# Kernel optimization log

Hardware: AMD Instinct MI355X
Metric: run time of the kernel (lower is better)

Reference implementation:

```python
import jax, jax.numpy as jnp
import numpy as np
import math

B, P, C = 8, 65536, 21
H, Wd, A = 128, 128, 4  # P == H*Wd*A
EMB, NID = 256, 1000
RATIO = 15
EMB_SCALE = math.sqrt(2) * math.log(NID - 1)


def setup_inputs() -> dict:
    key = jax.random.key(0)
    k1, k2, k3, k4, k5, k6 = jax.random.split(key, 6)
    confidence = jax.random.normal(k1, (B, P, C), dtype=jnp.float32)
    predicted_ids = jax.random.normal(k2, (B, H, Wd, EMB), dtype=jnp.float32)
    raw = jax.random.randint(k3, (B, P), 1, C)
    is_pos = jax.random.uniform(k4, (B, P)) < 0.02
    labels = jnp.where(is_pos, raw, 0).astype(jnp.int64)
    gt_ids = jax.random.randint(k5, (B, H, Wd, A), 0, NID).astype(jnp.int64)
    W = jax.random.normal(k6, (NID, EMB), dtype=jnp.float32) * 0.02
    b = jnp.zeros((NID,), dtype=jnp.float32)
    return {"confidence": confidence, "predicted_ids": predicted_ids,
            "labels": labels, "gt_ids": gt_ids, "W": W, "b": b}


def _hard_negative_mining(bg_loss, labels, ratio):
    # bg_loss: [B,P] = -log_softmax(confidence)[:, :, 0]
    pos = labels > 0
    num_pos = pos.sum(axis=1, keepdims=True)
    num_neg = num_pos * ratio
    l = jnp.where(pos, -jnp.inf, bg_loss)
    order = jnp.argsort(-l, axis=1)          # descending loss
    ranks = jnp.argsort(order, axis=1)       # rank of each prior
    neg = ranks < num_neg
    return pos | neg                          # [B,P]


def reference(confidence, predicted_ids, labels, gt_ids, W, b):
    # --- no_grad mining over all priors ---
    bg_loss = -jax.nn.log_softmax(confidence, axis=2)[:, :, 0]
    emb_mask = _hard_negative_mining(bg_loss, labels, RATIO)        # [B,P]
    # split to feature-map layout and reduce over anchors (mask.max(3))
    loc_mask = emb_mask.reshape(gt_ids.shape).max(axis=3)           # [B,H,W] bool
    gid = gt_ids.max(axis=3)                                        # [B,H,W]

    # --- normalize + scale + linear (computed densely, selection via mask) ---
    nrm = jnp.linalg.norm(predicted_ids, axis=-1, keepdims=True)
    pid = EMB_SCALE * predicted_ids / jnp.maximum(nrm, 1e-12)       # F.normalize
    logits = jnp.einsum('bhwe,ne->bhwn', pid, W) + b                # [B,H,W,NID]

    # --- masked cross-entropy, mean over selected & gid != -1 ---
    logp = jax.nn.log_softmax(logits, axis=-1)
    gid_safe = jnp.clip(gid, 0, NID - 1)
    ce = -jnp.take_along_axis(logp, gid_safe[..., None], axis=-1)[..., 0]
    valid = loc_mask & (gid >= 0)
    vf = valid.astype(ce.dtype)
    loss = (ce * vf).sum() / jnp.maximum(vf.sum(), 1.0)
    return loss
```

## Files before the change

kernel.cpp:

```cpp
#include <hip/hip_runtime.h>

typedef unsigned long long u64;
typedef __attribute__((ext_vector_type(8))) short short8;
typedef __attribute__((ext_vector_type(4))) float f32x4;

#define NB 8
#define PP 65536
#define CC 21
#define LOC_PER_B 16384
#define EMB_SCALE_F 9.76762622f
#define NID 1000

#define OFF_KEYS   0ull
#define OFF_HIST   4194304ull
#define OFF_WSWZ   6291456ull
#define OFF_STATE  6815744ull
#define ST_NUMPOS   0
#define ST_CANDCNT  32
#define ST_KTHHI    64
#define ST_KREM     96
#define ST_DONE     128
#define ST_KTH      160
#define ST_ACCUM    224
#define ST_WORDS    58

__device__ __forceinline__ unsigned short f2bf(float f) {
    unsigned u = __float_as_uint(f);
    u = (u + 0x7FFFu + ((u >> 16) & 1u)) >> 16;
    return (unsigned short)u;
}

__device__ __forceinline__ void gl_lds16(const void* g, void* l) {
    __builtin_amdgcn_global_load_lds((const __attribute__((address_space(1))) unsigned*)g,
                                     (__attribute__((address_space(3))) unsigned*)l, 16, 0, 0);
}

__global__ void k_init(unsigned* __restrict__ hist, unsigned* __restrict__ state) {
    int idx = blockIdx.x * 256 + threadIdx.x;
    if (idx < 524288) hist[idx] = 0u;
    int t = idx - 524288;
    if (t >= 0 && t < ST_WORDS) state[t] = 0u;
}

__global__ void k_wprep(const float* __restrict__ Wm, unsigned short* __restrict__ wswz) {
    int g = blockIdx.x * 256 + threadIdx.x;
    if (g >= 32768) return;
    int c    = g & 31;
    int row  = (g >> 5) & 63;
    int tile = g >> 11;
    int cls  = tile * 64 + row;
    int srcByte = (c << 4) ^ ((row & 7) << 4);
    ushort4 h0, h1;
    if (cls < NID) {
        const float* src = Wm + (size_t)cls * 256 + (srcByte >> 1);
        float4 a = *(const float4*)(src);
        float4 b = *(const float4*)(src + 4);
        h0.x = f2bf(a.x); h0.y = f2bf(a.y); h0.z = f2bf(a.z); h0.w = f2bf(a.w);
        h1.x = f2bf(b.x); h1.y = f2bf(b.y); h1.z = f2bf(b.z); h1.w = f2bf(b.w);
    } else {
        h0.x = h0.y = h0.z = h0.w = 0;
        h1.x = h1.y = h1.z = h1.w = 0;
    }
    ushort4* dst = (ushort4*)((char*)wswz + ((size_t)g << 4));
    dst[0] = h0; dst[1] = h1;
}

__global__ void k_keys(const float* __restrict__ conf, const int* __restrict__ labels,
                       u64* __restrict__ keys, int* __restrict__ numPos,
                       unsigned* __restrict__ hist) {
    int idx = blockIdx.x * 256 + threadIdx.x;
    int b = idx >> 16;
    int p = idx & 65535;
    const float* c = conf + (size_t)idx * CC;
    float x0 = c[0];
    float m = x0;
#pragma unroll
    for (int j = 1; j < CC; ++j) m = fmaxf(m, c[j]);
    float s = 0.f;
#pragma unroll
    for (int j = 0; j < CC; ++j) s += __expf(c[j] - m);
    float bg = m + __logf(s) - x0;
    bool pos = labels[idx] > 0;
    unsigned u = __float_as_uint(bg);
    u = (u & 0x80000000u) ? ~u : (u | 0x80000000u);
    u64 key = pos ? 0ull : ((((u64)u) << 32) | (u64)(0xFFFFFFFFu - (unsigned)p));
    keys[idx] = key;
    if (key) atomicAdd(&hist[(b << 16) + (int)(key >> 48)], 1u);
    u64 bal = __ballot(pos);
    if ((threadIdx.x & 63) == 0) {
        int cnt = __popcll(bal);
        if (cnt) atomicAdd(&numPos[b], cnt);
    }
}

__global__ void k_scan0(const unsigned* __restrict__ hist, const int* __restrict__ numPos,
                        unsigned* __restrict__ kthHi, unsigned* __restrict__ kRem,
                        unsigned* __restrict__ done, u64* __restrict__ kth) {
    int b = blockIdx.x, t = threadIdx.x;
    __shared__ unsigned s[1024];
    __shared__ unsigned sh_c, sh_kk;
    int np = numPos[b];
    long long kk64 = (long long)np * 15;
    long long neg = (long long)PP - np;
    if (kk64 > neg) kk64 = neg;
    unsigned k = (unsigned)kk64;
    if (k == 0) { if (t == 0) { done[b] = 1u; kth[b] = ~0ull; } return; }
    const unsigned* h = hist + (b << 16);
    unsigned cs = 0;
    const uint4* hv = (const uint4*)(h + (t << 6));
#pragma unroll
    for (int j = 0; j < 16; ++j) { uint4 v = hv[j]; cs += v.x + v.y + v.z + v.w; }
    s[t] = cs; __syncthreads();
    for (int off = 1; off < 1024; off <<= 1) {
        unsigned v = (t + off < 1024) ? s[t + off] : 0u;
        __syncthreads(); s[t] += v; __syncthreads();
    }
    unsigned si = s[t];
    if (si >= k && si - cs < k) { sh_c = (unsigned)t; sh_kk = k - (si - cs); }
    __syncthreads();
    if (t < 64) {
        unsigned c = sh_c, kk = sh_kk;
        unsigned bin = h[(c << 6) + t];
        unsigned sfx = bin;
        for (int off = 1; off < 64; off <<= 1) {
            unsigned v = __shfl_down(sfx, off, 64);
            if (t + off < 64) sfx += v;
        }
        if (sfx >= kk && sfx - bin < kk) {
            kthHi[b] = (c << 6) | (unsigned)t;
            kRem[b]  = kk - (sfx - bin);
        }
    }
}

__global__ void k_compact(const u64* __restrict__ keys, const unsigned* __restrict__ kthHi,
                          const unsigned* __restrict__ done, u64* __restrict__ cand,
                          unsigned* __restrict__ candCnt) {
    int idx = blockIdx.x * 256 + threadIdx.x;
    int b = idx >> 16;
    if (done[b]) return;
    u64 key = keys[idx];
    if ((unsigned)(key >> 48) == kthHi[b]) {
        unsigned pos = atomicAdd(&candCnt[b], 1u);
        if (pos < 32768u) cand[((size_t)b << 15) + pos] = key;
    }
}

__global__ void k_select2(const u64* __restrict__ cand, const unsigned* __restrict__ candCnt,
                          const unsigned* __restrict__ kthHi, const unsigned* __restrict__ kRem,
                          const unsigned* __restrict__ done, u64* __restrict__ kth) {
    int b = blockIdx.x, t = threadIdx.x;
    if (done[b]) return;
    __shared__ unsigned wh[4][256];
    __shared__ unsigned s[256];
    __shared__ u64 sh_pref;
    __shared__ unsigned sh_kk;
    int wv = t >> 6;
    unsigned n = candCnt[b]; if (n > 32768u) n = 32768u;
    if (t == 0) { sh_pref = 0ull; sh_kk = kRem[b]; }
    __syncthreads();
    const u64* cb = cand + ((size_t)b << 15);
    for (int pass = 0; pass < 6; ++pass) {
        int shift = 40 - 8 * pass;
        wh[0][t] = 0u; wh[1][t] = 0u; wh[2][t] = 0u; wh[3][t] = 0u;
        __syncthreads();
        u64 pref = sh_pref; unsigned kk = sh_kk;
        u64 himask = (~((1ull << (shift + 8)) - 1ull)) & 0x0000FFFFFFFFFFFFull;
        for (unsigned i = t; i < n; i += 256) {
            u64 kv = cb[i] & 0x0000FFFFFFFFFFFFull;
            if ((kv & himask) == pref)
                atomicAdd(&wh[wv][(unsigned)(kv >> shift) & 255u], 1u);
        }
        __syncthreads();
        unsigned hsum = wh[0][t] + wh[1][t] + wh[2][t] + wh[3][t];
        s[t] = hsum; __syncthreads();
        for (int off = 1; off < 256; off <<= 1) {
            unsigned v = (t + off < 256) ? s[t + off] : 0u;
            __syncthreads(); s[t] += v; __syncthreads();
        }
        unsigned si = s[t];
        if (si >= kk && si - hsum < kk) {
            sh_pref = pref | ((u64)t << shift);
            sh_kk = kk - (si - hsum);
        }
        __syncthreads();
    }
    if (t == 0) kth[b] = ((u64)kthHi[b] << 48) | sh_pref;
}

__launch_bounds__(256, 2)
__global__ void k_ce(const float* __restrict__ pid, const int* __restrict__ labels,
                     const int* __restrict__ gt, const unsigned short* __restrict__ wswz,
                     const float* __restrict__ bias, const u64* __restrict__ keys,
                     const u64* __restrict__ kth_, const unsigned* __restrict__ done_,
                     float* __restrict__ accum) {
    __shared__ __align__(16) char Ws[65536];
    __shared__ __align__(16) float biasLds[1024];
    __shared__ int gid_s[128];
    __shared__ unsigned mask_s[128];
    __shared__ float fsum[128];
    __shared__ float fgl[128];

    int tid = threadIdx.x;
    int blk = blockIdx.x;
    int b = blk >> 7;
    int locBase = (blk & 127) << 7;
    int wv = tid >> 6, lane = tid & 63;

#pragma unroll
    for (int i = 0; i < 4; ++i) {
        int idx = tid + (i << 8);
        biasLds[idx] = (idx < NID) ? bias[idx] : -INFINITY;
    }

    const float4* Xg = (const float4*)pid + ((size_t)b * LOC_PER_B + (size_t)locBase) * 64;
    for (int it = 0; it < 32; ++it) {
        int r = (it << 2) + wv;
        float4 v = Xg[(size_t)r * 64 + lane];
        float ss = v.x * v.x + v.y * v.y + v.z * v.z + v.w * v.w;
#pragma unroll
        for (int o = 32; o >= 1; o >>= 1) ss += __shfl_xor(ss, o, 64);
        float sc = EMB_SCALE_F / fmaxf(sqrtf(ss), 1e-12f);
        ushort4 h;
        h.x = f2bf(v.x * sc); h.y = f2bf(v.y * sc);
        h.z = f2bf(v.z * sc); h.w = f2bf(v.w * sc);
        *(ushort4*)(Ws + r * 512 + (((lane << 3)) ^ ((r & 7) << 4))) = h;
    }

    if (tid < 128) {
        size_t pb = (size_t)b * PP + ((size_t)(locBase + tid) << 2);
        int g0 = gt[pb], g1 = gt[pb + 1], g2 = gt[pb + 2], g3 = gt[pb + 3];
        int gid = max(max(g0, g1), max(g2, g3));
        u64 kth = kth_[b];
        unsigned dn = done_[b];
        unsigned msk = 0;
#pragma unroll
        for (int a = 0; a < 4; ++a) {
            if (labels[pb + a] > 0 || (!dn && keys[pb + a] >= kth)) msk = 1u;
        }
        if (gid < 0) msk = 0;
        gid_s[tid] = min(max(gid, 0), NID - 1);
        mask_s[tid] = msk;
        fsum[tid] = 0.f;
        fgl[tid] = 0.f;
    }

    asm volatile("s_waitcnt lgkmcnt(0)" ::: "memory");
    asm volatile("s_barrier" ::: "memory");

    int wrow = (wv >> 1) << 5;
    int wcol = (wv & 1) << 5;
    int kb = (lane >> 4) << 4;
    short8 af[2][2][8];
#pragma unroll
    for (int p = 0; p < 2; ++p)
#pragma unroll
        for (int ci = 0; ci < 2; ++ci) {
            int r = (p << 6) + wrow + (ci << 4) + (lane & 15);
            int swz = (r & 7) << 4;
#pragma unroll
            for (int ks = 0; ks < 8; ++ks)
                af[p][ci][ks] = *(const short8*)(Ws + r * 512 + ((((ks << 6) + kb)) ^ swz));
        }
    asm volatile("s_waitcnt lgkmcnt(0)" ::: "memory");
    asm volatile("s_barrier" ::: "memory");

    const char* wg = (const char*)wswz;
    {
        const char* g0 = wg + (wv << 13) + (lane << 4);
        char* l0 = Ws + (wv << 13);
#pragma unroll
        for (int it = 0; it < 8; ++it) gl_lds16(g0 + (it << 10), l0 + (it << 10));
        const char* g1 = wg + 32768 + (wv << 13) + (lane << 4);
        char* l1 = Ws + 32768 + (wv << 13);
#pragma unroll
        for (int it = 0; it < 8; ++it) gl_lds16(g1 + (it << 10), l1 + (it << 10));
    }

    float runsum[16];
#pragma unroll
    for (int i = 0; i < 16; ++i) runsum[i] = 0.f;

    int rc0 = wcol + (lane & 15);
    int swzB = (rc0 & 7) << 4;
    int kbx = kb ^ (swzB & 48);
    int szh = swzB & 64;
    int rbase0 = rc0 * 512 + kbx;
    int rbase1 = (rc0 + 16) * 512 + kbx;

    for (int nt = 0; nt < 16; ++nt) {
        int p = nt & 1;
        if (nt < 15) asm volatile("s_waitcnt vmcnt(8)" ::: "memory");
        else         asm volatile("s_waitcnt vmcnt(0)" ::: "memory");
        asm volatile("s_barrier" ::: "memory");

        const char* Wp = Ws + (p << 15);
        f32x4 a00 = {0,0,0,0}, a01 = {0,0,0,0}, a10 = {0,0,0,0}, a11 = {0,0,0,0};
        f32x4 c00 = {0,0,0,0}, c01 = {0,0,0,0}, c10 = {0,0,0,0}, c11 = {0,0,0,0};
#pragma unroll
        for (int ks = 0; ks < 8; ++ks) {
            int o = ((ks << 6) ^ szh);
            short8 b0 = *(const short8*)(Wp + rbase0 + o);
            short8 b1 = *(const short8*)(Wp + rbase1 + o);
            a00 = __builtin_amdgcn_mfma_f32_16x16x32_bf16(af[0][0][ks], b0, a00, 0, 0, 0);
            a01 = __builtin_amdgcn_mfma_f32_16x16x32_bf16(af[0][0][ks], b1, a01, 0, 0, 0);
            a10 = __builtin_amdgcn_mfma_f32_16x16x32_bf16(af[0][1][ks], b0, a10, 0, 0, 0);
            a11 = __builtin_amdgcn_mfma_f32_16x16x32_bf16(af[0][1][ks], b1, a11, 0, 0, 0);
            c00 = __builtin_amdgcn_mfma_f32_16x16x32_bf16(af[1][0][ks], b0, c00, 0, 0, 0);
            c01 = __builtin_amdgcn_mfma_f32_16x16x32_bf16(af[1][0][ks], b1, c01, 0, 0, 0);
            c10 = __builtin_amdgcn_mfma_f32_16x16x32_bf16(af[1][1][ks], b0, c10, 0, 0, 0);
            c11 = __builtin_amdgcn_mfma_f32_16x16x32_bf16(af[1][1][ks], b1, c11, 0, 0, 0);
        }
        asm volatile("s_barrier" ::: "memory");

        if (nt < 14) {
            const char* gs = wg + ((size_t)(nt + 2) << 15) + (wv << 13) + (lane << 4);
            char* ls = Ws + (p << 15) + (wv << 13);
#pragma unroll
            for (int it = 0; it < 8; ++it) gl_lds16(gs + (it << 10), ls + (it << 10));
        }

        int n0 = nt << 6;
        float bl0 = biasLds[n0 + wcol + (lane & 15)];
        float bl1 = biasLds[n0 + wcol + 16 + (lane & 15)];
#pragma unroll
        for (int reg = 0; reg < 4; ++reg) {
            runsum[reg]      += __expf(a00[reg] + bl0) + __expf(a01[reg] + bl1);
            runsum[4 + reg]  += __expf(a10[reg] + bl0) + __expf(a11[reg] + bl1);
            runsum[8 + reg]  += __expf(c00[reg] + bl0) + __expf(c01[reg] + bl1);
            runsum[12 + reg] += __expf(c10[reg] + bl0) + __expf(c11[reg] + bl1);
        }
    }

    if ((wv & 1) == 0) {
#pragma unroll
        for (int p = 0; p < 2; ++p)
#pragma unroll
            for (int ci = 0; ci < 2; ++ci) {
                int r = (p << 6) + wrow + (ci << 4) + (lane & 15);
                int gid = gid_s[r];
                const char* wrp = (const char*)wswz + (size_t)gid * 512;
                int gswz = (gid & 7) << 4;
                float d = 0.f;
#pragma unroll
                for (int ks = 0; ks < 8; ++ks) {
                    short8 w8 = *(const short8*)(wrp + ((((ks << 6) + kb)) ^ gswz));
                    short8 a8 = af[p][ci][ks];
#pragma unroll
                    for (int j = 0; j < 8; ++j) {
                        float xa = __uint_as_float((unsigned)(unsigned short)a8[j] << 16);
                        float xw = __uint_as_float((unsigned)(unsigned short)w8[j] << 16);
                        d = fmaf(xa, xw, d);
                    }
                }
                d += __shfl_xor(d, 16, 64);
                d += __shfl_xor(d, 32, 64);
                if (lane < 16) fgl[r] = d + biasLds[gid];
            }
    }

#pragma unroll
    for (int o = 1; o <= 8; o <<= 1)
#pragma unroll
        for (int i = 0; i < 16; ++i) runsum[i] += __shfl_xor(runsum[i], o, 64);

    if ((lane & 15) == 0) {
        int rb = wrow + ((lane >> 4) << 2);
#pragma unroll
        for (int p = 0; p < 2; ++p)
#pragma unroll
            for (int reg = 0; reg < 4; ++reg) {
                atomicAdd(&fsum[(p << 6) + rb + reg],      runsum[p * 8 + reg]);
                atomicAdd(&fsum[(p << 6) + rb + 16 + reg], runsum[p * 8 + 4 + reg]);
            }
    }
    __syncthreads();

    if (tid < 128) {
        float ce = __logf(fsum[tid]) - fgl[tid];
        float mm = (float)mask_s[tid];
        float cs = ce * mm;
#pragma unroll
        for (int o = 1; o <= 32; o <<= 1) {
            cs += __shfl_xor(cs, o, 64);
            mm += __shfl_xor(mm, o, 64);
        }
        if (lane == 0) {
            atomicAdd(&accum[0], cs);
            atomicAdd(&accum[1], mm);
        }
    }
}

__global__ void k_fin(const float* __restrict__ accum, float* __restrict__ out) {
    out[0] = accum[0] / fmaxf(accum[1], 1.0f);
}

extern "C" void kernel_launch(void* const* d_in, const int* in_sizes, int n_in,
                              void* d_out, int out_size, void* d_ws, size_t ws_size,
                              hipStream_t stream) {
    (void)in_sizes; (void)n_in; (void)out_size; (void)ws_size;
    const float* conf   = (const float*)d_in[0];
    const float* pid    = (const float*)d_in[1];
    const int*   labels = (const int*)d_in[2];
    const int*   gt     = (const int*)d_in[3];
    const float* Wm     = (const float*)d_in[4];
    const float* bias   = (const float*)d_in[5];
    float* out = (float*)d_out;
    char* ws = (char*)d_ws;

    u64* keys           = (u64*)(ws + OFF_KEYS);
    unsigned* hist      = (unsigned*)(ws + OFF_HIST);
    u64* cand           = (u64*)(ws + OFF_HIST);
    unsigned short* wsw = (unsigned short*)(ws + OFF_WSWZ);
    char* st            = ws + OFF_STATE;
    int* numPos         = (int*)(st + ST_NUMPOS);
    unsigned* candCnt   = (unsigned*)(st + ST_CANDCNT);
    unsigned* kthHi     = (unsigned*)(st + ST_KTHHI);
    unsigned* kRem      = (unsigned*)(st + ST_KREM);
    unsigned* done      = (unsigned*)(st + ST_DONE);
    u64* kth            = (u64*)(st + ST_KTH);
    float* accum        = (float*)(st + ST_ACCUM);

    k_init   <<<2049, 256, 0, stream>>>(hist, (unsigned*)st);
    k_wprep  <<<128,  256, 0, stream>>>(Wm, wsw);
    k_keys   <<<2048, 256, 0, stream>>>(conf, labels, keys, numPos, hist);
    k_scan0  <<<8,   1024, 0, stream>>>(hist, numPos, kthHi, kRem, done, kth);
    k_compact<<<2048, 256, 0, stream>>>(keys, kthHi, done, cand, candCnt);
    k_select2<<<8,    256, 0, stream>>>(cand, candCnt, kthHi, kRem, done, kth);
    k_ce     <<<1024, 256, 0, stream>>>(pid, labels, gt, wsw, bias, keys, kth, done, accum);
    k_fin    <<<1, 1, 0, stream>>>(accum, out);
}
```

Before: 481.4 us.

## Restructure CE kernel tiling, fold norm scale into epilogue, stage keys input in LDS

Measured after the change: 608.0 us. 26.3% more time.

```diff
diff --git a/kernel.cpp b/kernel.cpp
--- a/kernel.cpp
+++ b/kernel.cpp
@@ -4,10 +4,8 @@
 typedef __attribute__((ext_vector_type(8))) short short8;
 typedef __attribute__((ext_vector_type(4))) float f32x4;
 
-#define NB 8
 #define PP 65536
 #define CC 21
-#define LOC_PER_B 16384
 #define EMB_SCALE_F 9.76762622f
 #define NID 1000
 
@@ -30,48 +28,57 @@
     return (unsigned short)u;
 }
 
+__device__ __forceinline__ float bf2f(short s) {
+    return __uint_as_float((unsigned)(unsigned short)s << 16);
+}
+
 __device__ __forceinline__ void gl_lds16(const void* g, void* l) {
     __builtin_amdgcn_global_load_lds((const __attribute__((address_space(1))) unsigned*)g,
                                      (__attribute__((address_space(3))) unsigned*)l, 16, 0, 0);
 }
 
-__global__ void k_init(unsigned* __restrict__ hist, unsigned* __restrict__ state) {
+__global__ void k_prep(const float* __restrict__ Wm, unsigned short* __restrict__ wswz,
+                       unsigned* __restrict__ hist, unsigned* __restrict__ state) {
     int idx = blockIdx.x * 256 + threadIdx.x;
-    if (idx < 524288) hist[idx] = 0u;
-    int t = idx - 524288;
-    if (t >= 0 && t < ST_WORDS) state[t] = 0u;
-}
-
-__global__ void k_wprep(const float* __restrict__ Wm, unsigned short* __restrict__ wswz) {
-    int g = blockIdx.x * 256 + threadIdx.x;
-    if (g >= 32768) return;
-    int c    = g & 31;
-    int row  = (g >> 5) & 63;
-    int tile = g >> 11;
-    int cls  = tile * 64 + row;
-    int srcByte = (c << 4) ^ ((row & 7) << 4);
-    ushort4 h0, h1;
-    if (cls < NID) {
-        const float* src = Wm + (size_t)cls * 256 + (srcByte >> 1);
-        float4 a = *(const float4*)(src);
-        float4 b = *(const float4*)(src + 4);
-        h0.x = f2bf(a.x); h0.y = f2bf(a.y); h0.z = f2bf(a.z); h0.w = f2bf(a.w);
-        h1.x = f2bf(b.x); h1.y = f2bf(b.y); h1.z = f2bf(b.z); h1.w = f2bf(b.w);
-    } else {
+    hist[idx] = 0u;
+    if (idx < ST_WORDS) state[idx] = 0u;
+    if (idx < 32768) {
+        int c    = idx & 31;
+        int row  = (idx >> 5) & 31;
+        int tile = idx >> 10;
+        int cls  = tile * 32 + row;
+        ushort4 h0, h1;
         h0.x = h0.y = h0.z = h0.w = 0;
         h1.x = h1.y = h1.z = h1.w = 0;
-    }
-    ushort4* dst = (ushort4*)((char*)wswz + ((size_t)g << 4));
-    dst[0] = h0; dst[1] = h1;
+        if (cls < NID) {
+            int srcByte = (c << 4) ^ ((row & 7) << 4);
+            const float* s = Wm + (size_t)cls * 256 + (srcByte >> 1);
+            float4 a = *(const float4*)s;
+            float4 b = *(const float4*)(s + 4);
+            h0.x = f2bf(a.x); h0.y = f2bf(a.y); h0.z = f2bf(a.z); h0.w = f2bf(a.w);
+            h1.x = f2bf(b.x); h1.y = f2bf(b.y); h1.z = f2bf(b.z); h1.w = f2bf(b.w);
+        }
+        ushort4* dst = (ushort4*)((char*)wswz + ((size_t)idx << 4));
+        dst[0] = h0; dst[1] = h1;
+    }
 }
 
 __global__ void k_keys(const float* __restrict__ conf, const int* __restrict__ labels,
                        u64* __restrict__ keys, int* __restrict__ numPos,
                        unsigned* __restrict__ hist) {
-    int idx = blockIdx.x * 256 + threadIdx.x;
+    __shared__ float cs[5376];
+    int tid = threadIdx.x, blk = blockIdx.x;
+    const float4* src = (const float4*)(conf + (size_t)blk * 5376);
+#pragma unroll
+    for (int it = 0; it < 6; ++it) {
+        int g = tid + (it << 8);
+        if (g < 1344) ((float4*)cs)[g] = src[g];
+    }
+    __syncthreads();
+    int idx = blk * 256 + tid;
     int b = idx >> 16;
     int p = idx & 65535;
-    const float* c = conf + (size_t)idx * CC;
+    const float* c = cs + tid * 21;
     float x0 = c[0];
     float m = x0;
 #pragma unroll
@@ -87,7 +94,7 @@
     keys[idx] = key;
     if (key) atomicAdd(&hist[(b << 16) + (int)(key >> 48)], 1u);
     u64 bal = __ballot(pos);
-    if ((threadIdx.x & 63) == 0) {
+    if ((tid & 63) == 0) {
         int cnt = __popcll(bal);
         if (cnt) atomicAdd(&numPos[b], cnt);
     }
@@ -188,16 +195,16 @@
     if (t == 0) kth[b] = ((u64)kthHi[b] << 48) | sh_pref;
 }
 
-__launch_bounds__(256, 2)
+__launch_bounds__(256, 4)
 __global__ void k_ce(const float* __restrict__ pid, const int* __restrict__ labels,
                      const int* __restrict__ gt, const unsigned short* __restrict__ wswz,
                      const float* __restrict__ bias, const u64* __restrict__ keys,
                      const u64* __restrict__ kth_, const unsigned* __restrict__ done_,
                      float* __restrict__ accum) {
-    __shared__ __align__(16) char Ws[65536];
-    __shared__ __align__(16) float biasLds[1024];
+    __shared__ __align__(16) char Ws[32768];
+    __shared__ float biasLds[1024];
     __shared__ int gid_s[128];
-    __shared__ unsigned mask_s[128];
+    __shared__ float mask_s[128];
     __shared__ float fsum[128];
     __shared__ float fgl[128];
 
@@ -206,26 +213,39 @@
     int b = blk >> 7;
     int locBase = (blk & 127) << 7;
     int wv = tid >> 6, lane = tid & 63;
-
-#pragma unroll
-    for (int i = 0; i < 4; ++i) {
-        int idx = tid + (i << 8);
-        biasLds[idx] = (idx < NID) ? bias[idx] : -INFINITY;
-    }
-
-    const float4* Xg = (const float4*)pid + ((size_t)b * LOC_PER_B + (size_t)locBase) * 64;
-    for (int it = 0; it < 32; ++it) {
-        int r = (it << 2) + wv;
-        float4 v = Xg[(size_t)r * 64 + lane];
-        float ss = v.x * v.x + v.y * v.y + v.z * v.z + v.w * v.w;
-#pragma unroll
-        for (int o = 32; o >= 1; o >>= 1) ss += __shfl_xor(ss, o, 64);
-        float sc = EMB_SCALE_F / fmaxf(sqrtf(ss), 1e-12f);
-        ushort4 h;
-        h.x = f2bf(v.x * sc); h.y = f2bf(v.y * sc);
-        h.z = f2bf(v.z * sc); h.w = f2bf(v.w * sc);
-        *(ushort4*)(Ws + r * 512 + (((lane << 3)) ^ ((r & 7) << 4))) = h;
-    }
+    int l15 = lane & 15, l4 = lane >> 4;
+    int kb = l4 << 4;
+
+    short8 af[2][8];
+    float rs[2];
+    const char* Xb = (const char*)pid + (((size_t)b * 16384 + (size_t)locBase) << 10);
+#pragma unroll
+    for (int ci = 0; ci < 2; ++ci) {
+        const char* xr = Xb + (((size_t)(wv * 32 + ci * 16 + l15)) << 10) + (l4 << 5);
+        float ss = 0.f;
+#pragma unroll
+        for (int ks = 0; ks < 8; ++ks) {
+            float4 a  = *(const float4*)(xr + (ks << 7));
+            float4 c2 = *(const float4*)(xr + (ks << 7) + 16);
+            ss += a.x*a.x + a.y*a.y + a.z*a.z + a.w*a.w
+                + c2.x*c2.x + c2.y*c2.y + c2.z*c2.z + c2.w*c2.w;
+            short8 v;
+            v[0] = (short)f2bf(a.x);  v[1] = (short)f2bf(a.y);
+            v[2] = (short)f2bf(a.z);  v[3] = (short)f2bf(a.w);
+            v[4] = (short)f2bf(c2.x); v[5] = (short)f2bf(c2.y);
+            v[6] = (short)f2bf(c2.z); v[7] = (short)f2bf(c2.w);
+            af[ci][ks] = v;
+        }
+        ss += __shfl_xor(ss, 16, 64);
+        ss += __shfl_xor(ss, 32, 64);
+        rs[ci] = EMB_SCALE_F / fmaxf(sqrtf(ss), 1e-12f);
+    }
+    float sc[2][4];
+#pragma unroll
+    for (int ci = 0; ci < 2; ++ci)
+#pragma unroll
+        for (int reg = 0; reg < 4; ++reg)
+            sc[ci][reg] = __shfl(rs[ci], (l4 << 2) + reg, 64);
 
     if (tid < 128) {
         size_t pb = (size_t)b * PP + ((size_t)(locBase + tid) << 2);
@@ -235,158 +255,122 @@
         unsigned dn = done_[b];
         unsigned msk = 0;
 #pragma unroll
-        for (int a = 0; a < 4; ++a) {
+        for (int a = 0; a < 4; ++a)
             if (labels[pb + a] > 0 || (!dn && keys[pb + a] >= kth)) msk = 1u;
-        }
         if (gid < 0) msk = 0;
         gid_s[tid] = min(max(gid, 0), NID - 1);
-        mask_s[tid] = msk;
-        fsum[tid] = 0.f;
-        fgl[tid] = 0.f;
+        mask_s[tid] = (float)msk;
+    }
+#pragma unroll
+    for (int i = 0; i < 4; ++i) {
+        int idx = tid + (i << 8);
+        biasLds[idx] = (idx < NID) ? bias[idx] : -INFINITY;
+    }
+
+    {
+        const char* g0 = (const char*)wswz + (wv << 12) + (lane << 4);
+        char* l0 = Ws + (wv << 12);
+#pragma unroll
+        for (int it = 0; it < 4; ++it) gl_lds16(g0 + (it << 10), l0 + (it << 10));
+#pragma unroll
+        for (int it = 0; it < 4; ++it) gl_lds16(g0 + 16384 + (it << 10), l0 + 16384 + (it << 10));
     }
 
     asm volatile("s_waitcnt lgkmcnt(0)" ::: "memory");
-    asm volatile("s_barrier" ::: "memory");
-
-    int wrow = (wv >> 1) << 5;
-    int wcol = (wv & 1) << 5;
-    int kb = (lane >> 4) << 4;
-    short8 af[2][2][8];
-#pragma unroll
-    for (int p = 0; p < 2; ++p)
-#pragma unroll
-        for (int ci = 0; ci < 2; ++ci) {
-            int r = (p << 6) + wrow + (ci << 4) + (lane & 15);
-            int swz = (r & 7) << 4;
-#pragma unroll
-            for (int ks = 0; ks < 8; ++ks)
-                af[p][ci][ks] = *(const short8*)(Ws + r * 512 + ((((ks << 6) + kb)) ^ swz));
-        }
-    asm volatile("s_waitcnt lgkmcnt(0)" ::: "memory");
-    asm volatile("s_barrier" ::: "memory");
-
-    const char* wg = (const char*)wswz;
-    {
-        const char* g0 = wg + (wv << 13) + (lane << 4);
-        char* l0 = Ws + (wv << 13);
-#pragma unroll
-        for (int it = 0; it < 8; ++it) gl_lds16(g0 + (it << 10), l0 + (it << 10));
-        const char* g1 = wg + 32768 + (wv << 13) + (lane << 4);
-        char* l1 = Ws + 32768 + (wv << 13);
-#pragma unroll
-        for (int it = 0; it < 8; ++it) gl_lds16(g1 + (it << 10), l1 + (it << 10));
-    }
-
-    float runsum[16];
-#pragma unroll
-    for (int i = 0; i < 16; ++i) runsum[i] = 0.f;
-
-    int rc0 = wcol + (lane & 15);
-    int swzB = (rc0 & 7) << 4;
-    int kbx = kb ^ (swzB & 48);
-    int szh = swzB & 64;
-    int rbase0 = rc0 * 512 + kbx;
-    int rbase1 = (rc0 + 16) * 512 + kbx;
-
-    for (int nt = 0; nt < 16; ++nt) {
-        int p = nt & 1;
-        if (nt < 15) asm volatile("s_waitcnt vmcnt(8)" ::: "memory");
-        else         asm volatile("s_waitcnt vmcnt(0)" ::: "memory");
+
+    float runsum[2][4];
+#pragma unroll
+    for (int ci = 0; ci < 2; ++ci)
+#pragma unroll
+        for (int reg = 0; reg < 4; ++reg) runsum[ci][reg] = 0.f;
+
+    int swz = (l15 & 7) << 4;
+    const char* r0base = Ws + l15 * 512;
+    const char* r1base = Ws + (l15 + 16) * 512;
+
+#pragma unroll 1
+    for (int nt = 0; nt < 32; ++nt) {
+        if (nt == 31) asm volatile("s_waitcnt vmcnt(0)" ::: "memory");
+        else          asm volatile("s_waitcnt vmcnt(4)" ::: "memory");
         asm volatile("s_barrier" ::: "memory");
-
-        const char* Wp = Ws + (p << 15);
+        int p = (nt & 1) << 14;
+
         f32x4 a00 = {0,0,0,0}, a01 = {0,0,0,0}, a10 = {0,0,0,0}, a11 = {0,0,0,0};
-        f32x4 c00 = {0,0,0,0}, c01 = {0,0,0,0}, c10 = {0,0,0,0}, c11 = {0,0,0,0};
 #pragma unroll
         for (int ks = 0; ks < 8; ++ks) {
-            int o = ((ks << 6) ^ szh);
-            short8 b0 = *(const short8*)(Wp + rbase0 + o);
-            short8 b1 = *(const short8*)(Wp + rbase1 + o);
-            a00 = __builtin_amdgcn_mfma_f32_16x16x32_bf16(af[0][0][ks], b0, a00, 0, 0, 0);
-            a01 = __builtin_amdgcn_mfma_f32_16x16x32_bf16(af[0][0][ks], b1, a01, 0, 0, 0);
-            a10 = __builtin_amdgcn_mfma_f32_16x16x32_bf16(af[0][1][ks], b0, a10, 0, 0, 0);
-            a11 = __builtin_amdgcn_mfma_f32_16x16x32_bf16(af[0][1][ks], b1, a11, 0, 0, 0);
-            c00 = __builtin_amdgcn_mfma_f32_16x16x32_bf16(af[1][0][ks], b0, c00, 0, 0, 0);
-            c01 = __builtin_amdgcn_mfma_f32_16x16x32_bf16(af[1][0][ks], b1, c01, 0, 0, 0);
-            c10 = __builtin_amdgcn_mfma_f32_16x16x32_bf16(af[1][1][ks], b0, c10, 0, 0, 0);
-            c11 = __builtin_amdgcn_mfma_f32_16x16x32_bf16(af[1][1][ks], b1, c11, 0, 0, 0);
+            int off = ((((ks << 6) + kb)) ^ swz) + p;
+            short8 b0 = *(const short8*)(r0base + off);
+            short8 b1 = *(const short8*)(r1base + off);
+            a00 = __builtin_amdgcn_mfma_f32_16x16x32_bf16(af[0][ks], b0, a00, 0, 0, 0);
+            a01 = __builtin_amdgcn_mfma_f32_16x16x32_bf16(af[0][ks], b1, a01, 0, 0, 0);
+            a10 = __builtin_amdgcn_mfma_f32_16x16x32_bf16(af[1][ks], b0, a10, 0, 0, 0);
+            a11 = __builtin_amdgcn_mfma_f32_16x16x32_bf16(af[1][ks], b1, a11, 0, 0, 0);
         }
         asm volatile("s_barrier" ::: "memory");
 
-        if (nt < 14) {
-            const char* gs = wg + ((size_t)(nt + 2) << 15) + (wv << 13) + (lane << 4);
-            char* ls = Ws + (p << 15) + (wv << 13);
-#pragma unroll
-            for (int it = 0; it < 8; ++it) gl_lds16(gs + (it << 10), ls + (it << 10));
-        }
-
-        int n0 = nt << 6;
-        float bl0 = biasLds[n0 + wcol + (lane & 15)];
-        float bl1 = biasLds[n0 + wcol + 16 + (lane & 15)];
+        if (nt < 30) {
+            const char* gs = (const char*)wswz + ((size_t)(nt + 2) << 14) + (wv << 12) + (lane << 4);
+            char* ls = Ws + p + (wv << 12);
+#pragma unroll
+            for (int it = 0; it < 4; ++it) gl_lds16(gs + (it << 10), ls + (it << 10));
+        }
+
+        float bl0 = biasLds[(nt << 5) + l15];
+        float bl1 = biasLds[(nt << 5) + 16 + l15];
 #pragma unroll
         for (int reg = 0; reg < 4; ++reg) {
-            runsum[reg]      += __expf(a00[reg] + bl0) + __expf(a01[reg] + bl1);
-            runsum[4 + reg]  += __expf(a10[reg] + bl0) + __expf(a11[reg] + bl1);
-            runsum[8 + reg]  += __expf(c00[reg] + bl0) + __expf(c01[reg] + bl1);
-            runsum[12 + reg] += __expf(c10[reg] + bl0) + __expf(c11[reg] + bl1);
-        }
-    }
-
-    if ((wv & 1) == 0) {
-#pragma unroll
-        for (int p = 0; p < 2; ++p)
-#pragma unroll
-            for (int ci = 0; ci < 2; ++ci) {
-                int r = (p << 6) + wrow + (ci << 4) + (lane & 15);
-                int gid = gid_s[r];
-                const char* wrp = (const char*)wswz + (size_t)gid * 512;
-                int gswz = (gid & 7) << 4;
-                float d = 0.f;
-#pragma unroll
-                for (int ks = 0; ks < 8; ++ks) {
-                    short8 w8 = *(const short8*)(wrp + ((((ks << 6) + kb)) ^ gswz));
-                    short8 a8 = af[p][ci][ks];
-#pragma unroll
-                    for (int j = 0; j < 8; ++j) {
-                        float xa = __uint_as_float((unsigned)(unsigned short)a8[j] << 16);
-                        float xw = __uint_as_float((unsigned)(unsigned short)w8[j] << 16);
-                        d = fmaf(xa, xw, d);
-                    }
-                }
-                d += __shfl_xor(d, 16, 64);
-                d += __shfl_xor(d, 32, 64);
-                if (lane < 16) fgl[r] = d + biasLds[gid];
-            }
+            runsum[0][reg] += __expf(fmaf(a00[reg], sc[0][reg], bl0))
+                            + __expf(fmaf(a01[reg], sc[0][reg], bl1));
+            runsum[1][reg] += __expf(fmaf(a10[reg], sc[1][reg], bl0))
+                            + __expf(fmaf(a11[reg], sc[1][reg], bl1));
+        }
     }
 
 #pragma unroll
     for (int o = 1; o <= 8; o <<= 1)
 #pragma unroll
-        for (int i = 0; i < 16; ++i) runsum[i] += __shfl_xor(runsum[i], o, 64);
-
-    if ((lane & 15) == 0) {
-        int rb = wrow + ((lane >> 4) << 2);
-#pragma unroll
-        for (int p = 0; p < 2; ++p)
-#pragma unroll
-            for (int reg = 0; reg < 4; ++reg) {
-                atomicAdd(&fsum[(p << 6) + rb + reg],      runsum[p * 8 + reg]);
-                atomicAdd(&fsum[(p << 6) + rb + 16 + reg], runsum[p * 8 + 4 + reg]);
-            }
+        for (int ci = 0; ci < 2; ++ci)
+#pragma unroll
+            for (int reg = 0; reg < 4; ++reg)
+                runsum[ci][reg] += __shfl_xor(runsum[ci][reg], o, 64);
+    if (l15 == 0) {
+#pragma unroll
+        for (int ci = 0; ci < 2; ++ci)
+#pragma unroll
+            for (int reg = 0; reg < 4; ++reg)
+                fsum[wv * 32 + ci * 16 + (l4 << 2) + reg] = runsum[ci][reg];
+    }
+
+#pragma unroll
+    for (int ci = 0; ci < 2; ++ci) {
+        int gid = gid_s[wv * 32 + ci * 16 + l15];
+        const char* wr = (const char*)wswz + ((size_t)(gid >> 5) << 14) + ((size_t)(gid & 31) << 9);
+        int gsw = (gid & 7) << 4;
+        float d = 0.f;
+#pragma unroll
+        for (int ks = 0; ks < 8; ++ks) {
+            short8 w8 = *(const short8*)(wr + ((((ks << 6) + kb)) ^ gsw));
+            short8 a8 = af[ci][ks];
+#pragma unroll
+            for (int j = 0; j < 8; ++j) d = fmaf(bf2f(a8[j]), bf2f(w8[j]), d);
+        }
+        d += __shfl_xor(d, 16, 64);
+        d += __shfl_xor(d, 32, 64);
+        if (lane < 16) fgl[wv * 32 + ci * 16 + lane] = fmaf(d, rs[ci], biasLds[gid]);
     }
     __syncthreads();
 
     if (tid < 128) {
         float ce = __logf(fsum[tid]) - fgl[tid];
-        float mm = (float)mask_s[tid];
-        float cs = ce * mm;
+        float mm = mask_s[tid];
+        float cs2 = ce * mm;
 #pragma unroll
         for (int o = 1; o <= 32; o <<= 1) {
-            cs += __shfl_xor(cs, o, 64);
-            mm += __shfl_xor(mm, o, 64);
+            cs2 += __shfl_xor(cs2, o, 64);
+            mm  += __shfl_xor(mm, o, 64);
         }
         if (lane == 0) {
-            atomicAdd(&accum[0], cs);
+            atomicAdd(&accum[0], cs2);
             atomicAdd(&accum[1], mm);
         }
     }
@@ -422,8 +406,7 @@
     u64* kth            = (u64*)(st + ST_KTH);
     float* accum        = (float*)(st + ST_ACCUM);
 
-    k_init   <<<2049, 256, 0, stream>>>(hist, (unsigned*)st);
-    k_wprep  <<<128,  256, 0, stream>>>(Wm, wsw);
+    k_prep   <<<2048, 256, 0, stream>>>(Wm, wsw, hist, (unsigned*)st);
     k_keys   <<<2048, 256, 0, stream>>>(conf, labels, keys, numPos, hist);
     k_scan0  <<<8,   1024, 0, stream>>>(hist, numPos, kthHi, kRem, done, kth);
     k_compact<<<2048, 256, 0, stream>>>(keys, kthHi, done, cand, candCnt);
```
